# Performance work log

Measured on AMD Instinct MI355X. Metric: run time of the kernel, lower is better.

The kernel has to match this reference:

```python
import jax, jax.numpy as jnp
import numpy as np


def setup_inputs() -> dict:
    key = jax.random.key(0)
    ks = jax.random.split(key, 8)
    B, N, M, H = 8192, 2048, 2048, 10
    return {
        "X": jax.random.normal(ks[0], (B, N), dtype=jnp.float32),
        "weight": jax.random.normal(ks[1], (N, M), dtype=jnp.float32),
        "W1": jax.random.normal(ks[2], (3, H), dtype=jnp.float32) * 0.5,
        "b1": jax.random.normal(ks[3], (H,), dtype=jnp.float32) * 0.1,
        "W2": jax.random.normal(ks[4], (H, H), dtype=jnp.float32) * 0.3,
        "b2": jax.random.normal(ks[5], (H,), dtype=jnp.float32) * 0.1,
        "W3": jax.random.normal(ks[6], (H, 1), dtype=jnp.float32) * 0.3,
        "b3": jax.random.normal(ks[7], (1,), dtype=jnp.float32) * 0.1,
    }


def reference(X, weight, W1, b1, W2, b2, W3, b3):
    # NCA local rule, vectorized over all (i, j) cells.
    # 'forward'  = mean of column j excluding row i  (leave-one-out col mean)
    # 'backward' = mean of row i excluding column j  (leave-one-out row mean)
    n, m = weight.shape
    col_sum = jnp.sum(weight, axis=0, keepdims=True)            # [1, m]
    row_sum = jnp.sum(weight, axis=1, keepdims=True)            # [n, 1]
    fwd_mean = (col_sum - weight) / jnp.float32(n - 1)          # [n, m]
    bwd_mean = (row_sum - weight) / jnp.float32(m - 1)          # [n, m]
    feats = jnp.stack([weight, fwd_mean, bwd_mean], axis=-1)    # [n, m, 3]
    # tiny 3 -> 10 -> 10 -> 1 MLP applied per cell
    h = jax.nn.relu(feats @ W1 + b1)                            # [n, m, 10]
    h = jax.nn.relu(h @ W2 + b2)                                # [n, m, 10]
    updates = (h @ W3 + b3)[..., 0]                             # [n, m]
    new_weight = weight + updates
    # forward: softmax(X @ W)
    return jax.nn.softmax(X @ new_weight, axis=-1)
```

## Files before the change

### kernel.cpp

```cpp
#include <hip/hip_runtime.h>
#include <hip/hip_bf16.h>


typedef int int4v __attribute__((ext_vector_type(4)));
typedef int int16v __attribute__((ext_vector_type(16)));

#define GK 2048
#define NROWS 2048
#define MCOLS 2048
#define NCHUNK 16

#define CS_BLOCKS 128
#define RS_BLOCKS 2048
__global__ __launch_bounds__(256) void pre_kernel(
    const float* __restrict__ X, const float* __restrict__ W,
    signed char* __restrict__ X1, signed char* __restrict__ X2,
    float* __restrict__ sx1,
    float* __restrict__ part, float* __restrict__ rowS) {
  const int bid = blockIdx.x;
  const int tid = threadIdx.x;

  if (bid < CS_BLOCKS) {
    int chunk = bid >> 3;
    int j = (bid & 7) * 256 + tid;
    int i0 = chunk * (NROWS / NCHUNK);
    float s = 0.f;
    for (int i = i0; i < i0 + NROWS / NCHUNK; ++i) s += W[(size_t)i * MCOLS + j];
    part[(size_t)chunk * MCOLS + j] = s;
    return;
  }
  if (bid < CS_BLOCKS + RS_BLOCKS) {
    int row = bid - CS_BLOCKS;
    const float4* p = (const float4*)(W + (size_t)row * MCOLS);
    float4 a = p[tid];
    float4 b = p[tid + 256];
    float v = (a.x + a.y) + (a.z + a.w) + (b.x + b.y) + (b.z + b.w);
    __shared__ float red[256];
    red[tid] = v;
    __syncthreads();
    for (int s = 128; s > 0; s >>= 1) {
      if (tid < s) red[tid] += red[tid + s];
      __syncthreads();
    }
    if (tid == 0) rowS[row] = red[0];
    return;
  }
  {
    int row = bid - CS_BLOCKS - RS_BLOCKS;
    const float4* xr = (const float4*)(X + (size_t)row * GK);
    float4 a = xr[tid * 2];
    float4 b = xr[tid * 2 + 1];
    float xs[8] = {a.x, a.y, a.z, a.w, b.x, b.y, b.z, b.w};
    float am = 0.f;
#pragma unroll
    for (int i = 0; i < 8; ++i) am = fmaxf(am, fabsf(xs[i]));
    const int lane = tid & 63, wv = tid >> 6;
#pragma unroll
    for (int off = 32; off > 0; off >>= 1)
      am = fmaxf(am, __shfl_xor(am, off));
    __shared__ float wred[4];
    if (lane == 0) wred[wv] = am;
    __syncthreads();
    float amax = fmaxf(fmaxf(wred[0], wred[1]), fmaxf(wred[2], wred[3]));
    float s1 = amax * (1.0f / 127.0f);
    float inv = 127.0f / amax;
    int q1[8], q2[8];
#pragma unroll
    for (int i = 0; i < 8; ++i) {
      q1[i] = (int)rintf(xs[i] * inv);
      float r = xs[i] - (float)q1[i] * s1;
      q2[i] = (int)rintf(r * (254.0f * inv));
    }
    unsigned lo1 = (q1[0] & 255) | ((q1[1] & 255) << 8) | ((q1[2] & 255) << 16) | ((q1[3] & 255) << 24);
    unsigned hi1 = (q1[4] & 255) | ((q1[5] & 255) << 8) | ((q1[6] & 255) << 16) | ((q1[7] & 255) << 24);
    unsigned lo2 = (q2[0] & 255) | ((q2[1] & 255) << 8) | ((q2[2] & 255) << 16) | ((q2[3] & 255) << 24);
    unsigned hi2 = (q2[4] & 255) | ((q2[5] & 255) << 8) | ((q2[6] & 255) << 16) | ((q2[7] & 255) << 24);
    ((uint2*)(X1 + (size_t)row * GK))[tid] = make_uint2(lo1, hi1);
    ((uint2*)(X2 + (size_t)row * GK))[tid] = make_uint2(lo2, hi2);
    if (tid == 0) sx1[row] = s1;
  }
}

__global__ __launch_bounds__(256) void nca_update_kernel(
    const float* __restrict__ W, const float* __restrict__ part,
    const float* __restrict__ rowS,
    const float* __restrict__ W1, const float* __restrict__ b1,
    const float* __restrict__ W2, const float* __restrict__ b2,
    const float* __restrict__ W3, const float* __restrict__ b3,
    float* __restrict__ Wt) {
  __shared__ float sW1[30], sb1[10], sW2[100], sb2[10], sW3[10], sb3;
  __shared__ float sColS[32];
  __shared__ float cred[NCHUNK][33];
  __shared__ float Tf[32][33];
  const int tid = threadIdx.x;
  const int i0 = blockIdx.y * 32;
  const int j0 = blockIdx.x * 32;

  if (tid < 30) sW1[tid] = W1[tid];
  if (tid < 10) { sb1[tid] = b1[tid]; sb2[tid] = b2[tid]; sW3[tid] = W3[tid]; }
  if (tid >= 32 && tid < 132) sW2[tid - 32] = W2[tid - 32];
  if (tid == 0) sb3 = b3[0];

  {
    int ch = tid >> 5;
    int jl = tid & 31;
    cred[ch][jl]     = part[(size_t)ch * MCOLS + j0 + jl];
    cred[ch + 8][jl] = part[(size_t)(ch + 8) * MCOLS + j0 + jl];
  }
  __syncthreads();
  if (tid < 32) {
    float s = 0.f;
#pragma unroll
    for (int c = 0; c < NCHUNK; ++c) s += cred[c][tid];
    sColS[tid] = s;
  }
  __syncthreads();

  const int r = tid >> 5;
  const int c = tid & 31;

  float w[4], fwd[4], bwd[4];
#pragma unroll
  for (int cell = 0; cell < 4; ++cell) {
    int il = r + 8 * cell;
    float wv = W[(size_t)(i0 + il) * MCOLS + j0 + c];
    w[cell] = wv;
    fwd[cell] = (sColS[c] - wv) * (1.0f / (float)(NROWS - 1));
    bwd[cell] = (rowS[i0 + il] - wv) * (1.0f / (float)(MCOLS - 1));
  }

  float h1[4][10];
#pragma unroll
  for (int o = 0; o < 10; ++o) {
    float w1a = sW1[o], w1b = sW1[10 + o], w1c = sW1[20 + o], bb = sb1[o];
#pragma unroll
    for (int cell = 0; cell < 4; ++cell) {
      float v = fmaf(w[cell], w1a, fmaf(fwd[cell], w1b, fmaf(bwd[cell], w1c, bb)));
      h1[cell][o] = fmaxf(v, 0.f);
    }
  }
  float u[4] = {sb3, sb3, sb3, sb3};
#pragma unroll
  for (int o = 0; o < 10; ++o) {
    float h2[4];
    float bb = sb2[o];
#pragma unroll
    for (int cell = 0; cell < 4; ++cell) h2[cell] = bb;
#pragma unroll
    for (int p = 0; p < 10; ++p) {
      float wv = sW2[p * 10 + o];
#pragma unroll
      for (int cell = 0; cell < 4; ++cell) h2[cell] = fmaf(h1[cell][p], wv, h2[cell]);
    }
    float w3 = sW3[o];
#pragma unroll
    for (int cell = 0; cell < 4; ++cell) u[cell] = fmaf(fmaxf(h2[cell], 0.f), w3, u[cell]);
  }

#pragma unroll
  for (int cell = 0; cell < 4; ++cell) {
    int il = r + 8 * cell;
    Tf[il][c] = w[cell] + u[cell];
  }
  __syncthreads();

  {
    int r2 = tid >> 4;
    int ic = (tid & 15) * 2;
#pragma unroll
    for (int half = 0; half < 2; ++half) {
      int jl = r2 + 16 * half;
      float2 v = make_float2(Tf[ic][jl], Tf[ic + 1][jl]);
      *(float2*)(&Wt[(size_t)(j0 + jl) * NROWS + i0 + ic]) = v;
    }
  }
}

__global__ __launch_bounds__(256) void bquant_kernel(
    const float* __restrict__ Wt, signed char* __restrict__ B1,
    signed char* __restrict__ B2, float* __restrict__ sw1) {
  const int row = blockIdx.x;
  const int tid = threadIdx.x;
  const float4* wr = (const float4*)(Wt + (size_t)row * GK);
  float4 a = wr[tid * 2];
  float4 b = wr[tid * 2 + 1];
  float xs[8] = {a.x, a.y, a.z, a.w, b.x, b.y, b.z, b.w};
  float am = 0.f;
#pragma unroll
  for (int i = 0; i < 8; ++i) am = fmaxf(am, fabsf(xs[i]));
  const int lane = tid & 63, wv = tid >> 6;
#pragma unroll
  for (int off = 32; off > 0; off >>= 1)
    am = fmaxf(am, __shfl_xor(am, off));
  __shared__ float wred[4];
  if (lane == 0) wred[wv] = am;
  __syncthreads();
  float amax = fmaxf(fmaxf(wred[0], wred[1]), fmaxf(wred[2], wred[3]));
  float s1 = amax * (1.0f / 127.0f);
  float inv = 127.0f / amax;
  int q1[8], q2[8];
#pragma unroll
  for (int i = 0; i < 8; ++i) {
    q1[i] = (int)rintf(xs[i] * inv);
    float r = xs[i] - (float)q1[i] * s1;
    q2[i] = (int)rintf(r * (254.0f * inv));
  }
  unsigned lo1 = (q1[0] & 255) | ((q1[1] & 255) << 8) | ((q1[2] & 255) << 16) | ((q1[3] & 255) << 24);
  unsigned hi1 = (q1[4] & 255) | ((q1[5] & 255) << 8) | ((q1[6] & 255) << 16) | ((q1[7] & 255) << 24);
  unsigned lo2 = (q2[0] & 255) | ((q2[1] & 255) << 8) | ((q2[2] & 255) << 16) | ((q2[3] & 255) << 24);
  unsigned hi2 = (q2[4] & 255) | ((q2[5] & 255) << 8) | ((q2[6] & 255) << 16) | ((q2[7] & 255) << 24);
  ((uint2*)(B1 + (size_t)row * GK))[tid] = make_uint2(lo1, hi1);
  ((uint2*)(B2 + (size_t)row * GK))[tid] = make_uint2(lo2, hi2);
  if (tid == 0) sw1[row] = s1;
}

__global__ __launch_bounds__(256, 2) void gemm_kernel(
    const signed char* __restrict__ X1, const signed char* __restrict__ X2,
    const signed char* __restrict__ B1, const signed char* __restrict__ B2,
    const float* __restrict__ sw1, float* __restrict__ C) {
  __shared__ __align__(16) char sL[32768];

  const int tid = threadIdx.x;
  const int lane = tid & 63;
  const int wave = tid >> 6;
  const int wr = wave >> 1;
  const int wc = wave & 1;

  const int bx = blockIdx.x;
  const int by = blockIdx.y;

  const signed char* A1g = X1 + (size_t)(by * 128) * GK;
  const signed char* A2g = X2 + (size_t)(by * 128) * GK;
  const signed char* B1g = B1 + (size_t)(bx * 128) * GK;
  const signed char* B2g = B2 + (size_t)(bx * 128) * GK;

  const int srow = lane >> 2;
  const int skof = ((lane & 3) ^ ((lane >> 3) & 3)) * 16;

  const int rl = lane & 15;
  const int fhalf = (lane >> 4) & 1;
  const int fck = lane >> 5;

  int aoff[2][2], boff[2][2];
#pragma unroll
  for (int t = 0; t < 2; ++t)
#pragma unroll
    for (int ks = 0; ks < 2; ++ks) {
      int c = 2 * ks + fck;
      int slot = 4 * rl + (c ^ ((rl >> 1) & 3));
      aoff[t][ks] = (wr * 4 + t * 2 + fhalf) * 1024 + slot * 16;
      boff[t][ks] = (wc * 4 + t * 2 + fhalf) * 1024 + slot * 16;
    }

  int16v acc_h[2][2], acc_c[2][2];
#pragma unroll
  for (int i = 0; i < 2; ++i)
#pragma unroll
    for (int j = 0; j < 2; ++j)
#pragma unroll
      for (int e = 0; e < 16; ++e) { acc_h[i][j][e] = 0; acc_c[i][j][e] = 0; }

  for (int k0 = 0; k0 < GK; k0 += 64) {
#pragma unroll
    for (int r = 0; r < 2; ++r) {
      int R = wave * 2 + r;
      size_t goff = (size_t)(R * 16 + srow) * GK + k0 + skof;
      int ldsoff = R * 1024;
      __builtin_amdgcn_global_load_lds(
          (const __attribute__((address_space(1))) void*)(A1g + goff),
          (__attribute__((address_space(3))) void*)(sL + ldsoff), 16, 0, 0);
      __builtin_amdgcn_global_load_lds(
          (const __attribute__((address_space(1))) void*)(A2g + goff),
          (__attribute__((address_space(3))) void*)(sL + 8192 + ldsoff), 16, 0, 0);
      __builtin_amdgcn_global_load_lds(
          (const __attribute__((address_space(1))) void*)(B1g + goff),
          (__attribute__((address_space(3))) void*)(sL + 16384 + ldsoff), 16, 0, 0);
      __builtin_amdgcn_global_load_lds(
          (const __attribute__((address_space(1))) void*)(B2g + goff),
          (__attribute__((address_space(3))) void*)(sL + 24576 + ldsoff), 16, 0, 0);
    }
    __syncthreads();

    int4v a1[2][2], a2[2][2];
#pragma unroll
    for (int mi = 0; mi < 2; ++mi)
#pragma unroll
      for (int ks = 0; ks < 2; ++ks) {
        a1[mi][ks] = *(const int4v*)(sL + aoff[mi][ks]);
        a2[mi][ks] = *(const int4v*)(sL + 8192 + aoff[mi][ks]);
      }
#pragma unroll
    for (int ni = 0; ni < 2; ++ni)
#pragma unroll
      for (int ks = 0; ks < 2; ++ks) {
        int4v b1f = *(const int4v*)(sL + 16384 + boff[ni][ks]);
        int4v b2f = *(const int4v*)(sL + 24576 + boff[ni][ks]);
#pragma unroll
        for (int mi = 0; mi < 2; ++mi) {
          acc_h[mi][ni] = __builtin_amdgcn_mfma_i32_32x32x32_i8(a1[mi][ks], b1f, acc_h[mi][ni], 0, 0, 0);
          acc_c[mi][ni] = __builtin_amdgcn_mfma_i32_32x32x32_i8(a1[mi][ks], b2f, acc_c[mi][ni], 0, 0, 0);
          acc_c[mi][ni] = __builtin_amdgcn_mfma_i32_32x32x32_i8(a2[mi][ks], b1f, acc_c[mi][ni], 0, 0, 0);
        }
      }
    __syncthreads();
  }

  const int ecol = lane & 31;
  const int erow = 4 * (lane >> 5);
#pragma unroll
  for (int ni = 0; ni < 2; ++ni) {
    int col = bx * 128 + wc * 64 + ni * 32 + ecol;
    float sw = sw1[col];
#pragma unroll
    for (int mi = 0; mi < 2; ++mi) {
#pragma unroll
      for (int reg = 0; reg < 16; ++reg) {
        int row = by * 128 + wr * 64 + mi * 32 + (reg & 3) + 8 * (reg >> 2) + erow;
        float v = (float)acc_h[mi][ni][reg] + (float)acc_c[mi][ni][reg] * (1.0f / 254.0f);
        C[(size_t)row * 2048 + col] = v * sw;
      }
    }
  }
}

__global__ __launch_bounds__(256) void softmax_kernel(
    float* __restrict__ C, const float* __restrict__ sx1) {
  const int lane = threadIdx.x & 63;
  const int wv = threadIdx.x >> 6;
  const int row = blockIdx.x * 4 + wv;
  const float sx = sx1[row];
  float4* p = (float4*)(C + (size_t)row * MCOLS);

  float4 v[8];
#pragma unroll
  for (int j = 0; j < 8; ++j) {
    v[j] = p[j * 64 + lane];
    v[j].x *= sx; v[j].y *= sx; v[j].z *= sx; v[j].w *= sx;
  }

  float vmax = -3.4e38f;
#pragma unroll
  for (int j = 0; j < 8; ++j)
    vmax = fmaxf(vmax, fmaxf(fmaxf(v[j].x, v[j].y), fmaxf(v[j].z, v[j].w)));
#pragma unroll
  for (int off = 32; off > 0; off >>= 1)
    vmax = fmaxf(vmax, __shfl_xor(vmax, off));

  float sum = 0.f;
#pragma unroll
  for (int j = 0; j < 8; ++j) {
    v[j].x = __expf(v[j].x - vmax);
    v[j].y = __expf(v[j].y - vmax);
    v[j].z = __expf(v[j].z - vmax);
    v[j].w = __expf(v[j].w - vmax);
    sum += (v[j].x + v[j].y) + (v[j].z + v[j].w);
  }
#pragma unroll
  for (int off = 32; off > 0; off >>= 1)
    sum += __shfl_xor(sum, off);
  float inv = 1.0f / sum;

#pragma unroll
  for (int j = 0; j < 8; ++j) {
    v[j].x *= inv; v[j].y *= inv; v[j].z *= inv; v[j].w *= inv;
    p[j * 64 + lane] = v[j];
  }
}

extern "C" void kernel_launch(void* const* d_in, const int* in_sizes, int n_in,
                              void* d_out, int out_size, void* d_ws, size_t ws_size,
                              hipStream_t stream) {
  const float* X      = (const float*)d_in[0];
  const float* weight = (const float*)d_in[1];
  const float* W1     = (const float*)d_in[2];
  const float* b1     = (const float*)d_in[3];
  const float* W2     = (const float*)d_in[4];
  const float* b2     = (const float*)d_in[5];
  const float* W3     = (const float*)d_in[6];
  const float* b3     = (const float*)d_in[7];
  float* out = (float*)d_out;

  const int N = 2048, M = 2048;
  const int Bdim = in_sizes[0] / N;

  float* rowS = (float*)d_ws;
  float* part = rowS + 2048;
  float* sx1  = part + NCHUNK * 2048;
  float* sw1  = sx1 + 8192;
  float* Wt   = sw1 + 2048;
  signed char* X1 = (signed char*)(Wt + (size_t)M * N);
  signed char* X2 = X1 + (size_t)Bdim * N;
  signed char* B1q = X2 + (size_t)Bdim * N;
  signed char* B2q = B1q + (size_t)M * N;

  pre_kernel<<<CS_BLOCKS + RS_BLOCKS + Bdim, 256, 0, stream>>>(
      X, weight, X1, X2, sx1, part, rowS);

  nca_update_kernel<<<dim3(M / 32, N / 32), 256, 0, stream>>>(
      weight, part, rowS, W1, b1, W2, b2, W3, b3, Wt);

  bquant_kernel<<<M, 256, 0, stream>>>(Wt, B1q, B2q, sw1);

  gemm_kernel<<<dim3(M / 128, Bdim / 128), 256, 0, stream>>>(
      X1, X2, B1q, B2q, sw1, out);

  softmax_kernel<<<Bdim / 4, 256, 0, stream>>>(out, sx1);
}
```

Baseline: 289.3 us.

## Restructure int8 GEMM into 256x128 tiles with triple-buffered LDS prefetch

The GEMM block grows to 512 threads and a 256x128 output tile. The single-buffer load-then-compute loop becomes a three-stage LDS ring that prefetches two K-steps ahead, with global loads interleaved between MFMA quadrants and s_setprio raised around the MFMA groups. The aim is to hide global-to-LDS latency behind compute and to reuse each B tile across more rows. In exchange it uses 144KB of LDS per block, which limits occupancy, and it relies on hand-placed waitcnt and barrier sequencing that must be exactly right.

```diff
diff --git a/kernel.cpp b/kernel.cpp
--- a/kernel.cpp
+++ b/kernel.cpp
@@ -214,11 +214,39 @@
   if (tid == 0) sw1[row] = s1;
 }
 
-__global__ __launch_bounds__(256, 2) void gemm_kernel(
+#define BM 256
+#define BN 128
+#define BK 64
+#define NT (GK / BK)
+#define BUFSZ 49152
+
+__device__ __forceinline__ void glds16(const signed char* g, char* l) {
+  __builtin_amdgcn_global_load_lds(
+      (const __attribute__((address_space(1))) void*)g,
+      (__attribute__((address_space(3))) void*)l, 16, 0, 0);
+}
+
+#define QUAD(mi, ni)                                                           \
+  {                                                                            \
+    acc_h[mi][ni] = __builtin_amdgcn_mfma_i32_32x32x32_i8(                     \
+        a1f[mi][0], b1f[ni][0], acc_h[mi][ni], 0, 0, 0);                       \
+    acc_c[mi][ni] = __builtin_amdgcn_mfma_i32_32x32x32_i8(                     \
+        a1f[mi][0], b2f[ni][0], acc_c[mi][ni], 0, 0, 0);                       \
+    acc_c[mi][ni] = __builtin_amdgcn_mfma_i32_32x32x32_i8(                     \
+        a2f[mi][0], b1f[ni][0], acc_c[mi][ni], 0, 0, 0);                       \
+    acc_h[mi][ni] = __builtin_amdgcn_mfma_i32_32x32x32_i8(                     \
+        a1f[mi][1], b1f[ni][1], acc_h[mi][ni], 0, 0, 0);                       \
+    acc_c[mi][ni] = __builtin_amdgcn_mfma_i32_32x32x32_i8(                     \
+        a1f[mi][1], b2f[ni][1], acc_c[mi][ni], 0, 0, 0);                       \
+    acc_c[mi][ni] = __builtin_amdgcn_mfma_i32_32x32x32_i8(                     \
+        a2f[mi][1], b1f[ni][1], acc_c[mi][ni], 0, 0, 0);                       \
+  }
+
+__global__ __launch_bounds__(512, 2) void gemm_kernel(
     const signed char* __restrict__ X1, const signed char* __restrict__ X2,
     const signed char* __restrict__ B1, const signed char* __restrict__ B2,
     const float* __restrict__ sw1, float* __restrict__ C) {
-  __shared__ __align__(16) char sL[32768];
+  __shared__ __align__(16) char sL[3 * BUFSZ];
 
   const int tid = threadIdx.x;
   const int lane = tid & 63;
@@ -229,27 +257,28 @@
   const int bx = blockIdx.x;
   const int by = blockIdx.y;
 
-  const signed char* A1g = X1 + (size_t)(by * 128) * GK;
-  const signed char* A2g = X2 + (size_t)(by * 128) * GK;
-  const signed char* B1g = B1 + (size_t)(bx * 128) * GK;
-  const signed char* B2g = B2 + (size_t)(bx * 128) * GK;
+  const signed char* A1g = X1 + (size_t)(by * BM) * GK;
+  const signed char* A2g = X2 + (size_t)(by * BM) * GK;
+  const signed char* B1g = B1 + (size_t)(bx * BN) * GK;
+  const signed char* B2g = B2 + (size_t)(bx * BN) * GK;
 
   const int srow = lane >> 2;
-  const int skof = ((lane & 3) ^ ((lane >> 3) & 3)) * 16;
+  const int schk = (lane & 3) ^ ((lane >> 3) & 3);
+  const size_t qoff = (size_t)(wave * 16 + srow) * GK + schk * 16;
+  const int wds = wave * 1024;
 
   const int rl = lane & 15;
-  const int fhalf = (lane >> 4) & 1;
-  const int fck = lane >> 5;
-
+  const int bhalf = (lane >> 4) & 1;
+  const int kck = lane >> 5;
   int aoff[2][2], boff[2][2];
 #pragma unroll
-  for (int t = 0; t < 2; ++t)
+  for (int mi = 0; mi < 2; ++mi)
 #pragma unroll
     for (int ks = 0; ks < 2; ++ks) {
-      int c = 2 * ks + fck;
+      int c = 2 * ks + kck;
       int slot = 4 * rl + (c ^ ((rl >> 1) & 3));
-      aoff[t][ks] = (wr * 4 + t * 2 + fhalf) * 1024 + slot * 16;
-      boff[t][ks] = (wc * 4 + t * 2 + fhalf) * 1024 + slot * 16;
+      aoff[mi][ks] = (wr * 4 + mi * 2 + bhalf) * 1024 + slot * 16;
+      boff[mi][ks] = 32768 + (wc * 4 + mi * 2 + bhalf) * 1024 + slot * 16;
     }
 
   int16v acc_h[2][2], acc_c[2][2];
@@ -260,64 +289,103 @@
 #pragma unroll
       for (int e = 0; e < 16; ++e) { acc_h[i][j][e] = 0; acc_c[i][j][e] = 0; }
 
-  for (int k0 = 0; k0 < GK; k0 += 64) {
-#pragma unroll
-    for (int r = 0; r < 2; ++r) {
-      int R = wave * 2 + r;
-      size_t goff = (size_t)(R * 16 + srow) * GK + k0 + skof;
-      int ldsoff = R * 1024;
-      __builtin_amdgcn_global_load_lds(
-          (const __attribute__((address_space(1))) void*)(A1g + goff),
-          (__attribute__((address_space(3))) void*)(sL + ldsoff), 16, 0, 0);
-      __builtin_amdgcn_global_load_lds(
-          (const __attribute__((address_space(1))) void*)(A2g + goff),
-          (__attribute__((address_space(3))) void*)(sL + 8192 + ldsoff), 16, 0, 0);
-      __builtin_amdgcn_global_load_lds(
-          (const __attribute__((address_space(1))) void*)(B1g + goff),
-          (__attribute__((address_space(3))) void*)(sL + 16384 + ldsoff), 16, 0, 0);
-      __builtin_amdgcn_global_load_lds(
-          (const __attribute__((address_space(1))) void*)(B2g + goff),
-          (__attribute__((address_space(3))) void*)(sL + 24576 + ldsoff), 16, 0, 0);
-    }
-    __syncthreads();
-
-    int4v a1[2][2], a2[2][2];
-#pragma unroll
-    for (int mi = 0; mi < 2; ++mi)
-#pragma unroll
-      for (int ks = 0; ks < 2; ++ks) {
-        a1[mi][ks] = *(const int4v*)(sL + aoff[mi][ks]);
-        a2[mi][ks] = *(const int4v*)(sL + 8192 + aoff[mi][ks]);
-      }
-#pragma unroll
-    for (int ni = 0; ni < 2; ++ni)
-#pragma unroll
-      for (int ks = 0; ks < 2; ++ks) {
-        int4v b1f = *(const int4v*)(sL + 16384 + boff[ni][ks]);
-        int4v b2f = *(const int4v*)(sL + 24576 + boff[ni][ks]);
-#pragma unroll
-        for (int mi = 0; mi < 2; ++mi) {
-          acc_h[mi][ni] = __builtin_amdgcn_mfma_i32_32x32x32_i8(a1[mi][ks], b1f, acc_h[mi][ni], 0, 0, 0);
-          acc_c[mi][ni] = __builtin_amdgcn_mfma_i32_32x32x32_i8(a1[mi][ks], b2f, acc_c[mi][ni], 0, 0, 0);
-          acc_c[mi][ni] = __builtin_amdgcn_mfma_i32_32x32x32_i8(a2[mi][ks], b1f, acc_c[mi][ni], 0, 0, 0);
-        }
-      }
-    __syncthreads();
+#pragma unroll
+  for (int t = 0; t < 2; ++t) {
+    char* wb = sL + t * BUFSZ;
+    const size_t k0 = (size_t)t * BK;
+    glds16(A1g + qoff + k0, wb + wds);
+    glds16(A1g + qoff + (size_t)128 * GK + k0, wb + 8192 + wds);
+    glds16(A2g + qoff + k0, wb + 16384 + wds);
+    glds16(A2g + qoff + (size_t)128 * GK + k0, wb + 24576 + wds);
+    glds16(B1g + qoff + k0, wb + 32768 + wds);
+    glds16(B2g + qoff + k0, wb + 40960 + wds);
+  }
+
+  const char* sbuf = sL;
+  char* wbuf = sL + 2 * BUFSZ;
+
+  int4v a1f[2][2], a2f[2][2], b1f[2][2], b2f[2][2];
+
+#pragma unroll 1
+  for (int kt = 0; kt < NT; ++kt) {
+    if (kt + 1 < NT) asm volatile("s_waitcnt vmcnt(6)" ::: "memory");
+    else             asm volatile("s_waitcnt vmcnt(0)" ::: "memory");
+    __builtin_amdgcn_s_barrier();
+
+    const size_t k2 = (size_t)(kt + 2) * BK;
+    const bool pf = (kt + 2 < NT);
+
+#pragma unroll
+    for (int ks = 0; ks < 2; ++ks) {
+      a1f[0][ks] = *(const int4v*)(sbuf + aoff[0][ks]);
+      a2f[0][ks] = *(const int4v*)(sbuf + aoff[0][ks] + 16384);
+      b1f[0][ks] = *(const int4v*)(sbuf + boff[0][ks]);
+      b2f[0][ks] = *(const int4v*)(sbuf + boff[0][ks] + 8192);
+    }
+    if (pf) {
+      glds16(A1g + qoff + k2, wbuf + wds);
+      glds16(A1g + qoff + (size_t)128 * GK + k2, wbuf + 8192 + wds);
+    }
+    __builtin_amdgcn_s_barrier();
+    asm volatile("s_waitcnt lgkmcnt(0)" ::: "memory");
+    __builtin_amdgcn_s_setprio(1);
+    QUAD(0, 0);
+    __builtin_amdgcn_s_setprio(0);
+    __builtin_amdgcn_s_barrier();
+
+#pragma unroll
+    for (int ks = 0; ks < 2; ++ks) {
+      b1f[1][ks] = *(const int4v*)(sbuf + boff[1][ks]);
+      b2f[1][ks] = *(const int4v*)(sbuf + boff[1][ks] + 8192);
+    }
+    if (pf) {
+      glds16(A2g + qoff + k2, wbuf + 16384 + wds);
+      glds16(A2g + qoff + (size_t)128 * GK + k2, wbuf + 24576 + wds);
+    }
+    __builtin_amdgcn_s_barrier();
+    asm volatile("s_waitcnt lgkmcnt(0)" ::: "memory");
+    __builtin_amdgcn_s_setprio(1);
+    QUAD(0, 1);
+    __builtin_amdgcn_s_setprio(0);
+    __builtin_amdgcn_s_barrier();
+
+#pragma unroll
+    for (int ks = 0; ks < 2; ++ks) {
+      a1f[1][ks] = *(const int4v*)(sbuf + aoff[1][ks]);
+      a2f[1][ks] = *(const int4v*)(sbuf + aoff[1][ks] + 16384);
+    }
+    if (pf) {
+      glds16(B1g + qoff + k2, wbuf + 32768 + wds);
+      glds16(B2g + qoff + k2, wbuf + 40960 + wds);
+    }
+    __builtin_amdgcn_s_barrier();
+    asm volatile("s_waitcnt lgkmcnt(0)" ::: "memory");
+    __builtin_amdgcn_s_setprio(1);
+    QUAD(1, 1);
+    __builtin_amdgcn_s_setprio(0);
+    __builtin_amdgcn_s_barrier();
+
+    __builtin_amdgcn_s_setprio(1);
+    QUAD(1, 0);
+    __builtin_amdgcn_s_setprio(0);
+
+    sbuf += BUFSZ; if (sbuf == sL + 3 * BUFSZ) sbuf = sL;
+    wbuf += BUFSZ; if (wbuf == sL + 3 * BUFSZ) wbuf = sL;
   }
 
   const int ecol = lane & 31;
   const int erow = 4 * (lane >> 5);
 #pragma unroll
   for (int ni = 0; ni < 2; ++ni) {
-    int col = bx * 128 + wc * 64 + ni * 32 + ecol;
+    int col = bx * BN + wc * 64 + ni * 32 + ecol;
     float sw = sw1[col];
 #pragma unroll
     for (int mi = 0; mi < 2; ++mi) {
 #pragma unroll
       for (int reg = 0; reg < 16; ++reg) {
-        int row = by * 128 + wr * 64 + mi * 32 + (reg & 3) + 8 * (reg >> 2) + erow;
+        int row = by * BM + wr * 64 + mi * 32 + (reg & 3) + 8 * (reg >> 2) + erow;
         float v = (float)acc_h[mi][ni][reg] + (float)acc_c[mi][ni][reg] * (1.0f / 254.0f);
-        C[(size_t)row * 2048 + col] = v * sw;
+        C[(size_t)row * MCOLS + col] = v * sw;
       }
     }
   }
@@ -401,7 +469,7 @@
 
   bquant_kernel<<<M, 256, 0, stream>>>(Wt, B1q, B2q, sw1);
 
-  gemm_kernel<<<dim3(M / 128, Bdim / 128), 256, 0, stream>>>(
+  gemm_kernel<<<dim3(M / BN, Bdim / BM), 512, 0, stream>>>(
       X1, X2, B1q, B2q, sw1, out);
 
   softmax_kernel<<<Bdim / 4, 256, 0, stream>>>(out, sx1);
```

Measured after the change: 288.7 us. About the same (-0.2%).

## Pipeline int8 GEMM with 4-stage LDS ring and register double-buffered fragments

Applied to the files above, without the earlier changes.

The int8 split-precision GEMM becomes a software pipeline. A 4-buffer LDS ring keeps tiles prefetched three K-steps ahead with direct global-to-LDS loads, one barrier per step and explicit vmcnt/lgkmcnt waits. Register fragments are double-buffered so the next step's ds_reads overlap the current MFMAs, and each wave loads one of the four operand streams. This costs 128KB of LDS and one block per CU instead of two. The NCA update kernel also reads the MLP weights directly from global memory instead of staging them in shared memory.

```diff
diff --git a/kernel.cpp b/kernel.cpp
--- a/kernel.cpp
+++ b/kernel.cpp
@@ -88,7 +88,6 @@
     const float* __restrict__ W2, const float* __restrict__ b2,
     const float* __restrict__ W3, const float* __restrict__ b3,
     float* __restrict__ Wt) {
-  __shared__ float sW1[30], sb1[10], sW2[100], sb2[10], sW3[10], sb3;
   __shared__ float sColS[32];
   __shared__ float cred[NCHUNK][33];
   __shared__ float Tf[32][33];
@@ -96,11 +95,6 @@
   const int i0 = blockIdx.y * 32;
   const int j0 = blockIdx.x * 32;
 
-  if (tid < 30) sW1[tid] = W1[tid];
-  if (tid < 10) { sb1[tid] = b1[tid]; sb2[tid] = b2[tid]; sW3[tid] = W3[tid]; }
-  if (tid >= 32 && tid < 132) sW2[tid - 32] = W2[tid - 32];
-  if (tid == 0) sb3 = b3[0];
-
   {
     int ch = tid >> 5;
     int jl = tid & 31;
@@ -132,27 +126,28 @@
   float h1[4][10];
 #pragma unroll
   for (int o = 0; o < 10; ++o) {
-    float w1a = sW1[o], w1b = sW1[10 + o], w1c = sW1[20 + o], bb = sb1[o];
+    float w1a = W1[o], w1b = W1[10 + o], w1c = W1[20 + o], bb = b1[o];
 #pragma unroll
     for (int cell = 0; cell < 4; ++cell) {
       float v = fmaf(w[cell], w1a, fmaf(fwd[cell], w1b, fmaf(bwd[cell], w1c, bb)));
       h1[cell][o] = fmaxf(v, 0.f);
     }
   }
-  float u[4] = {sb3, sb3, sb3, sb3};
+  const float b3v = b3[0];
+  float u[4] = {b3v, b3v, b3v, b3v};
 #pragma unroll
   for (int o = 0; o < 10; ++o) {
     float h2[4];
-    float bb = sb2[o];
+    float bb = b2[o];
 #pragma unroll
     for (int cell = 0; cell < 4; ++cell) h2[cell] = bb;
 #pragma unroll
     for (int p = 0; p < 10; ++p) {
-      float wv = sW2[p * 10 + o];
+      float wv = W2[p * 10 + o];
 #pragma unroll
       for (int cell = 0; cell < 4; ++cell) h2[cell] = fmaf(h1[cell][p], wv, h2[cell]);
     }
-    float w3 = sW3[o];
+    float w3 = W3[o];
 #pragma unroll
     for (int cell = 0; cell < 4; ++cell) u[cell] = fmaf(fmaxf(h2[cell], 0.f), w3, u[cell]);
   }
@@ -214,11 +209,99 @@
   if (tid == 0) sw1[row] = s1;
 }
 
-__global__ __launch_bounds__(256, 2) void gemm_kernel(
+#define BM 128
+#define BN 128
+#define BK 64
+#define NT (GK / BK)
+#define BUFSZ 32768
+#define SROWSZ ((size_t)16 * GK)
+
+__device__ __forceinline__ void glds16(const signed char* g, char* l) {
+  __builtin_amdgcn_global_load_lds(
+      (const __attribute__((address_space(1))) void*)g,
+      (__attribute__((address_space(3))) void*)l, 16, 0, 0);
+}
+
+__device__ __forceinline__ int4v ds_read128(const char* p) {
+  int4v r;
+  asm volatile("ds_read_b128 %0, %1"
+               : "=v"(r)
+               : "v"((const __attribute__((address_space(3))) char*)p));
+  return r;
+}
+
+#define MFMA_I8 __builtin_amdgcn_mfma_i32_32x32x32_i8
+
+#define RD16(NX, rb_)                                                          \
+  NX##a1[0][0] = ds_read128((rb_) + aoff[0][0]);                               \
+  NX##a1[0][1] = ds_read128((rb_) + aoff[0][1]);                               \
+  NX##a1[1][0] = ds_read128((rb_) + aoff[1][0]);                               \
+  NX##a1[1][1] = ds_read128((rb_) + aoff[1][1]);                               \
+  NX##a2[0][0] = ds_read128((rb_) + aoff[0][0] + 8192);                        \
+  NX##a2[0][1] = ds_read128((rb_) + aoff[0][1] + 8192);                        \
+  NX##a2[1][0] = ds_read128((rb_) + aoff[1][0] + 8192);                        \
+  NX##a2[1][1] = ds_read128((rb_) + aoff[1][1] + 8192);                        \
+  NX##b1[0][0] = ds_read128((rb_) + boff[0][0]);                               \
+  NX##b1[0][1] = ds_read128((rb_) + boff[0][1]);                               \
+  NX##b1[1][0] = ds_read128((rb_) + boff[1][0]);                               \
+  NX##b1[1][1] = ds_read128((rb_) + boff[1][1]);                               \
+  NX##b2[0][0] = ds_read128((rb_) + boff[0][0] + 8192);                        \
+  NX##b2[0][1] = ds_read128((rb_) + boff[0][1] + 8192);                        \
+  NX##b2[1][0] = ds_read128((rb_) + boff[1][0] + 8192);                        \
+  NX##b2[1][1] = ds_read128((rb_) + boff[1][1] + 8192);
+
+#define MM12(CUR, ks)                                                          \
+  acc_h[0][0] = MFMA_I8(CUR##a1[0][ks], CUR##b1[0][ks], acc_h[0][0], 0, 0, 0); \
+  acc_h[0][1] = MFMA_I8(CUR##a1[0][ks], CUR##b1[1][ks], acc_h[0][1], 0, 0, 0); \
+  acc_h[1][0] = MFMA_I8(CUR##a1[1][ks], CUR##b1[0][ks], acc_h[1][0], 0, 0, 0); \
+  acc_h[1][1] = MFMA_I8(CUR##a1[1][ks], CUR##b1[1][ks], acc_h[1][1], 0, 0, 0); \
+  acc_c[0][0] = MFMA_I8(CUR##a1[0][ks], CUR##b2[0][ks], acc_c[0][0], 0, 0, 0); \
+  acc_c[0][1] = MFMA_I8(CUR##a1[0][ks], CUR##b2[1][ks], acc_c[0][1], 0, 0, 0); \
+  acc_c[1][0] = MFMA_I8(CUR##a1[1][ks], CUR##b2[0][ks], acc_c[1][0], 0, 0, 0); \
+  acc_c[1][1] = MFMA_I8(CUR##a1[1][ks], CUR##b2[1][ks], acc_c[1][1], 0, 0, 0); \
+  acc_c[0][0] = MFMA_I8(CUR##a2[0][ks], CUR##b1[0][ks], acc_c[0][0], 0, 0, 0); \
+  acc_c[0][1] = MFMA_I8(CUR##a2[0][ks], CUR##b1[1][ks], acc_c[0][1], 0, 0, 0); \
+  acc_c[1][0] = MFMA_I8(CUR##a2[1][ks], CUR##b1[0][ks], acc_c[1][0], 0, 0, 0); \
+  acc_c[1][1] = MFMA_I8(CUR##a2[1][ks], CUR##b1[1][ks], acc_c[1][1], 0, 0, 0);
+
+#define STAGE8(wb_, gp_)                                                       \
+  glds16((gp_) + 0 * SROWSZ, (wb_) + 0 * 1024 + lane * 16);                    \
+  glds16((gp_) + 1 * SROWSZ, (wb_) + 1 * 1024 + lane * 16);                    \
+  glds16((gp_) + 2 * SROWSZ, (wb_) + 2 * 1024 + lane * 16);                    \
+  glds16((gp_) + 3 * SROWSZ, (wb_) + 3 * 1024 + lane * 16);                    \
+  glds16((gp_) + 4 * SROWSZ, (wb_) + 4 * 1024 + lane * 16);                    \
+  glds16((gp_) + 5 * SROWSZ, (wb_) + 5 * 1024 + lane * 16);                    \
+  glds16((gp_) + 6 * SROWSZ, (wb_) + 6 * 1024 + lane * 16);                    \
+  glds16((gp_) + 7 * SROWSZ, (wb_) + 7 * 1024 + lane * 16);
+
+#define STEP(i, CUR, NXT)                                                      \
+  {                                                                            \
+    if ((i) + 2 < NT) asm volatile("s_waitcnt vmcnt(8)" ::: "memory");         \
+    else              asm volatile("s_waitcnt vmcnt(0)" ::: "memory");         \
+    __builtin_amdgcn_s_barrier();                                              \
+    if ((i) + 1 < NT) {                                                        \
+      const char* rb_ = sL + (((i) + 1) & 3) * BUFSZ;                          \
+      RD16(NXT, rb_);                                                          \
+    }                                                                          \
+    if ((i) + 3 < NT) {                                                        \
+      char* wb_ = sL + (((i) + 3) & 3) * BUFSZ + wave * 8192;                  \
+      const signed char* gp_ = gw + (size_t)((i) + 3) * BK;                    \
+      STAGE8(wb_, gp_);                                                        \
+    }                                                                          \
+    if ((i) + 1 < NT) asm volatile("s_waitcnt lgkmcnt(15)" ::: "memory");      \
+    else              asm volatile("s_waitcnt lgkmcnt(0)" ::: "memory");       \
+    __builtin_amdgcn_sched_barrier(0);                                         \
+    __builtin_amdgcn_s_setprio(1);                                             \
+    MM12(CUR, 0);                                                              \
+    MM12(CUR, 1);                                                              \
+    __builtin_amdgcn_s_setprio(0);                                             \
+  }
+
+__global__ __launch_bounds__(256, 1) void gemm_kernel(
     const signed char* __restrict__ X1, const signed char* __restrict__ X2,
     const signed char* __restrict__ B1, const signed char* __restrict__ B2,
     const float* __restrict__ sw1, float* __restrict__ C) {
-  __shared__ __align__(16) char sL[32768];
+  __shared__ __align__(16) char sL[4 * BUFSZ];
 
   const int tid = threadIdx.x;
   const int lane = tid & 63;
@@ -229,27 +312,29 @@
   const int bx = blockIdx.x;
   const int by = blockIdx.y;
 
-  const signed char* A1g = X1 + (size_t)(by * 128) * GK;
-  const signed char* A2g = X2 + (size_t)(by * 128) * GK;
-  const signed char* B1g = B1 + (size_t)(bx * 128) * GK;
-  const signed char* B2g = B2 + (size_t)(bx * 128) * GK;
+  const signed char* A1g = X1 + (size_t)(by * BM) * GK;
+  const signed char* A2g = X2 + (size_t)(by * BM) * GK;
+  const signed char* B1g = B1 + (size_t)(bx * BN) * GK;
+  const signed char* B2g = B2 + (size_t)(bx * BN) * GK;
 
   const int srow = lane >> 2;
-  const int skof = ((lane & 3) ^ ((lane >> 3) & 3)) * 16;
+  const int schk = (lane & 3) ^ ((lane >> 3) & 3);
+  const signed char* gw =
+      (wave == 0 ? A1g : wave == 1 ? A2g : wave == 2 ? B1g : B2g) +
+      (size_t)srow * GK + schk * 16;
 
   const int rl = lane & 15;
   const int fhalf = (lane >> 4) & 1;
   const int fck = lane >> 5;
-
   int aoff[2][2], boff[2][2];
 #pragma unroll
-  for (int t = 0; t < 2; ++t)
+  for (int mi = 0; mi < 2; ++mi)
 #pragma unroll
     for (int ks = 0; ks < 2; ++ks) {
       int c = 2 * ks + fck;
       int slot = 4 * rl + (c ^ ((rl >> 1) & 3));
-      aoff[t][ks] = (wr * 4 + t * 2 + fhalf) * 1024 + slot * 16;
-      boff[t][ks] = (wc * 4 + t * 2 + fhalf) * 1024 + slot * 16;
+      aoff[mi][ks] = (wr * 4 + mi * 2 + fhalf) * 1024 + slot * 16;
+      boff[mi][ks] = 16384 + (wc * 4 + mi * 2 + fhalf) * 1024 + slot * 16;
     }
 
   int16v acc_h[2][2], acc_c[2][2];
@@ -260,64 +345,38 @@
 #pragma unroll
       for (int e = 0; e < 16; ++e) { acc_h[i][j][e] = 0; acc_c[i][j][e] = 0; }
 
-  for (int k0 = 0; k0 < GK; k0 += 64) {
-#pragma unroll
-    for (int r = 0; r < 2; ++r) {
-      int R = wave * 2 + r;
-      size_t goff = (size_t)(R * 16 + srow) * GK + k0 + skof;
-      int ldsoff = R * 1024;
-      __builtin_amdgcn_global_load_lds(
-          (const __attribute__((address_space(1))) void*)(A1g + goff),
-          (__attribute__((address_space(3))) void*)(sL + ldsoff), 16, 0, 0);
-      __builtin_amdgcn_global_load_lds(
-          (const __attribute__((address_space(1))) void*)(A2g + goff),
-          (__attribute__((address_space(3))) void*)(sL + 8192 + ldsoff), 16, 0, 0);
-      __builtin_amdgcn_global_load_lds(
-          (const __attribute__((address_space(1))) void*)(B1g + goff),
-          (__attribute__((address_space(3))) void*)(sL + 16384 + ldsoff), 16, 0, 0);
-      __builtin_amdgcn_global_load_lds(
-          (const __attribute__((address_space(1))) void*)(B2g + goff),
-          (__attribute__((address_space(3))) void*)(sL + 24576 + ldsoff), 16, 0, 0);
-    }
-    __syncthreads();
-
-    int4v a1[2][2], a2[2][2];
-#pragma unroll
-    for (int mi = 0; mi < 2; ++mi)
-#pragma unroll
-      for (int ks = 0; ks < 2; ++ks) {
-        a1[mi][ks] = *(const int4v*)(sL + aoff[mi][ks]);
-        a2[mi][ks] = *(const int4v*)(sL + 8192 + aoff[mi][ks]);
-      }
-#pragma unroll
-    for (int ni = 0; ni < 2; ++ni)
-#pragma unroll
-      for (int ks = 0; ks < 2; ++ks) {
-        int4v b1f = *(const int4v*)(sL + 16384 + boff[ni][ks]);
-        int4v b2f = *(const int4v*)(sL + 24576 + boff[ni][ks]);
-#pragma unroll
-        for (int mi = 0; mi < 2; ++mi) {
-          acc_h[mi][ni] = __builtin_amdgcn_mfma_i32_32x32x32_i8(a1[mi][ks], b1f, acc_h[mi][ni], 0, 0, 0);
-          acc_c[mi][ni] = __builtin_amdgcn_mfma_i32_32x32x32_i8(a1[mi][ks], b2f, acc_c[mi][ni], 0, 0, 0);
-          acc_c[mi][ni] = __builtin_amdgcn_mfma_i32_32x32x32_i8(a2[mi][ks], b1f, acc_c[mi][ni], 0, 0, 0);
-        }
-      }
-    __syncthreads();
+  int4v s0_a1[2][2], s0_a2[2][2], s0_b1[2][2], s0_b2[2][2];
+  int4v s1_a1[2][2], s1_a2[2][2], s1_b1[2][2], s1_b2[2][2];
+
+#pragma unroll
+  for (int t = 0; t < 3; ++t) {
+    char* wb = sL + t * BUFSZ + wave * 8192;
+    const signed char* gp = gw + (size_t)t * BK;
+    STAGE8(wb, gp);
+  }
+  asm volatile("s_waitcnt vmcnt(16)" ::: "memory");
+  __builtin_amdgcn_s_barrier();
+  RD16(s0_, sL);
+
+#pragma unroll 1
+  for (int i = 0; i < NT; i += 2) {
+    STEP(i, s0_, s1_);
+    STEP(i + 1, s1_, s0_);
   }
 
   const int ecol = lane & 31;
   const int erow = 4 * (lane >> 5);
 #pragma unroll
   for (int ni = 0; ni < 2; ++ni) {
-    int col = bx * 128 + wc * 64 + ni * 32 + ecol;
+    int col = bx * BN + wc * 64 + ni * 32 + ecol;
     float sw = sw1[col];
 #pragma unroll
     for (int mi = 0; mi < 2; ++mi) {
 #pragma unroll
       for (int reg = 0; reg < 16; ++reg) {
-        int row = by * 128 + wr * 64 + mi * 32 + (reg & 3) + 8 * (reg >> 2) + erow;
+        int row = by * BM + wr * 64 + mi * 32 + (reg & 3) + 8 * (reg >> 2) + erow;
         float v = (float)acc_h[mi][ni][reg] + (float)acc_c[mi][ni][reg] * (1.0f / 254.0f);
-        C[(size_t)row * 2048 + col] = v * sw;
+        C[(size_t)row * MCOLS + col] = v * sw;
       }
     }
   }
@@ -401,7 +460,7 @@
 
   bquant_kernel<<<M, 256, 0, stream>>>(Wt, B1q, B2q, sw1);
 
-  gemm_kernel<<<dim3(M / 128, Bdim / 128), 256, 0, stream>>>(
+  gemm_kernel<<<dim3(M / BN, Bdim / BM), 256, 0, stream>>>(
       X1, X2, B1q, B2q, sw1, out);
 
   softmax_kernel<<<Bdim / 4, 256, 0, stream>>>(out, sx1);
```

Result: slower. 317.5 us (+9.8%).

## Pre-swizzle int8 operands into MFMA fragment layout and stream GEMM from registers

Applied to the files above, without the earlier changes.

The quantization kernels now handle one row per wave and write int8 data directly in MFMA-fragment order. The GEMM can then load its operands straight from global memory into registers with a double-buffered register prefetch, with no LDS staging or barriers. The GEMM tile grows to 256x128 with 512 threads, and the NCA kernel reads the MLP weights directly instead of staging them in shared memory. Without LDS, operand reuse across waves now relies on L2/L1 caching, which may raise global memory traffic.

```diff
diff --git a/kernel.cpp b/kernel.cpp
--- a/kernel.cpp
+++ b/kernel.cpp
@@ -46,38 +46,48 @@
     return;
   }
   {
-    int row = bid - CS_BLOCKS - RS_BLOCKS;
-    const float4* xr = (const float4*)(X + (size_t)row * GK);
-    float4 a = xr[tid * 2];
-    float4 b = xr[tid * 2 + 1];
-    float xs[8] = {a.x, a.y, a.z, a.w, b.x, b.y, b.z, b.w};
+    int rb = bid - CS_BLOCKS - RS_BLOCKS;
+    const int lane = tid & 63, wv = tid >> 6;
+    const int row = rb * 4 + wv;
+    const float4* xr = (const float4*)(X + (size_t)row * GK) + lane * 8;
+    float xs[32];
+#pragma unroll
+    for (int i = 0; i < 8; ++i) {
+      float4 t = xr[i];
+      xs[i * 4 + 0] = t.x; xs[i * 4 + 1] = t.y;
+      xs[i * 4 + 2] = t.z; xs[i * 4 + 3] = t.w;
+    }
     float am = 0.f;
 #pragma unroll
-    for (int i = 0; i < 8; ++i) am = fmaxf(am, fabsf(xs[i]));
-    const int lane = tid & 63, wv = tid >> 6;
+    for (int i = 0; i < 32; ++i) am = fmaxf(am, fabsf(xs[i]));
 #pragma unroll
     for (int off = 32; off > 0; off >>= 1)
       am = fmaxf(am, __shfl_xor(am, off));
-    __shared__ float wred[4];
-    if (lane == 0) wred[wv] = am;
-    __syncthreads();
-    float amax = fmaxf(fmaxf(wred[0], wred[1]), fmaxf(wred[2], wred[3]));
-    float s1 = amax * (1.0f / 127.0f);
-    float inv = 127.0f / amax;
-    int q1[8], q2[8];
-#pragma unroll
-    for (int i = 0; i < 8; ++i) {
-      q1[i] = (int)rintf(xs[i] * inv);
-      float r = xs[i] - (float)q1[i] * s1;
-      q2[i] = (int)rintf(r * (254.0f * inv));
-    }
-    unsigned lo1 = (q1[0] & 255) | ((q1[1] & 255) << 8) | ((q1[2] & 255) << 16) | ((q1[3] & 255) << 24);
-    unsigned hi1 = (q1[4] & 255) | ((q1[5] & 255) << 8) | ((q1[6] & 255) << 16) | ((q1[7] & 255) << 24);
-    unsigned lo2 = (q2[0] & 255) | ((q2[1] & 255) << 8) | ((q2[2] & 255) << 16) | ((q2[3] & 255) << 24);
-    unsigned hi2 = (q2[4] & 255) | ((q2[5] & 255) << 8) | ((q2[6] & 255) << 16) | ((q2[7] & 255) << 24);
-    ((uint2*)(X1 + (size_t)row * GK))[tid] = make_uint2(lo1, hi1);
-    ((uint2*)(X2 + (size_t)row * GK))[tid] = make_uint2(lo2, hi2);
-    if (tid == 0) sx1[row] = s1;
+    float s1 = am * (1.0f / 127.0f);
+    float inv = 127.0f / am;
+    unsigned w1[8], w2[8];
+#pragma unroll
+    for (int i = 0; i < 8; ++i) { w1[i] = 0u; w2[i] = 0u; }
+#pragma unroll
+    for (int i = 0; i < 32; ++i) {
+      int q1 = (int)rintf(xs[i] * inv);
+      float r = xs[i] - (float)q1 * s1;
+      int q2 = (int)rintf(r * (254.0f * inv));
+      w1[i >> 2] |= (unsigned)(q1 & 255) << ((i & 3) * 8);
+      w2[i >> 2] |= (unsigned)(q2 & 255) << ((i & 3) * 8);
+    }
+    const int m32 = row >> 5, ml = row & 31;
+    int4v* d1 = (int4v*)X1 + ((size_t)m32 * 64 + lane) * 64;
+    int4v* d2 = (int4v*)X2 + ((size_t)m32 * 64 + lane) * 64;
+    int4v v1lo = {(int)w1[0], (int)w1[1], (int)w1[2], (int)w1[3]};
+    int4v v1hi = {(int)w1[4], (int)w1[5], (int)w1[6], (int)w1[7]};
+    int4v v2lo = {(int)w2[0], (int)w2[1], (int)w2[2], (int)w2[3]};
+    int4v v2hi = {(int)w2[4], (int)w2[5], (int)w2[6], (int)w2[7]};
+    d1[ml]      = v1lo;
+    d1[ml + 32] = v1hi;
+    d2[ml]      = v2lo;
+    d2[ml + 32] = v2hi;
+    if (lane == 0) sx1[row] = s1;
   }
 }
 
@@ -88,7 +98,6 @@
     const float* __restrict__ W2, const float* __restrict__ b2,
     const float* __restrict__ W3, const float* __restrict__ b3,
     float* __restrict__ Wt) {
-  __shared__ float sW1[30], sb1[10], sW2[100], sb2[10], sW3[10], sb3;
   __shared__ float sColS[32];
   __shared__ float cred[NCHUNK][33];
   __shared__ float Tf[32][33];
@@ -96,11 +105,6 @@
   const int i0 = blockIdx.y * 32;
   const int j0 = blockIdx.x * 32;
 
-  if (tid < 30) sW1[tid] = W1[tid];
-  if (tid < 10) { sb1[tid] = b1[tid]; sb2[tid] = b2[tid]; sW3[tid] = W3[tid]; }
-  if (tid >= 32 && tid < 132) sW2[tid - 32] = W2[tid - 32];
-  if (tid == 0) sb3 = b3[0];
-
   {
     int ch = tid >> 5;
     int jl = tid & 31;
@@ -132,27 +136,28 @@
   float h1[4][10];
 #pragma unroll
   for (int o = 0; o < 10; ++o) {
-    float w1a = sW1[o], w1b = sW1[10 + o], w1c = sW1[20 + o], bb = sb1[o];
+    float w1a = W1[o], w1b = W1[10 + o], w1c = W1[20 + o], bb = b1[o];
 #pragma unroll
     for (int cell = 0; cell < 4; ++cell) {
       float v = fmaf(w[cell], w1a, fmaf(fwd[cell], w1b, fmaf(bwd[cell], w1c, bb)));
       h1[cell][o] = fmaxf(v, 0.f);
     }
   }
-  float u[4] = {sb3, sb3, sb3, sb3};
+  const float b3v = b3[0];
+  float u[4] = {b3v, b3v, b3v, b3v};
 #pragma unroll
   for (int o = 0; o < 10; ++o) {
     float h2[4];
-    float bb = sb2[o];
+    float bb = b2[o];
 #pragma unroll
     for (int cell = 0; cell < 4; ++cell) h2[cell] = bb;
 #pragma unroll
     for (int p = 0; p < 10; ++p) {
-      float wv = sW2[p * 10 + o];
+      float wv = W2[p * 10 + o];
 #pragma unroll
       for (int cell = 0; cell < 4; ++cell) h2[cell] = fmaf(h1[cell][p], wv, h2[cell]);
     }
-    float w3 = sW3[o];
+    float w3 = W3[o];
 #pragma unroll
     for (int cell = 0; cell < 4; ++cell) u[cell] = fmaf(fmaxf(h2[cell], 0.f), w3, u[cell]);
   }
@@ -179,47 +184,83 @@
 __global__ __launch_bounds__(256) void bquant_kernel(
     const float* __restrict__ Wt, signed char* __restrict__ B1,
     signed char* __restrict__ B2, float* __restrict__ sw1) {
-  const int row = blockIdx.x;
   const int tid = threadIdx.x;
-  const float4* wr = (const float4*)(Wt + (size_t)row * GK);
-  float4 a = wr[tid * 2];
-  float4 b = wr[tid * 2 + 1];
-  float xs[8] = {a.x, a.y, a.z, a.w, b.x, b.y, b.z, b.w};
+  const int lane = tid & 63, wv = tid >> 6;
+  const int row = blockIdx.x * 4 + wv;
+  const float4* wr = (const float4*)(Wt + (size_t)row * GK) + lane * 8;
+  float xs[32];
+#pragma unroll
+  for (int i = 0; i < 8; ++i) {
+    float4 t = wr[i];
+    xs[i * 4 + 0] = t.x; xs[i * 4 + 1] = t.y;
+    xs[i * 4 + 2] = t.z; xs[i * 4 + 3] = t.w;
+  }
   float am = 0.f;
 #pragma unroll
-  for (int i = 0; i < 8; ++i) am = fmaxf(am, fabsf(xs[i]));
-  const int lane = tid & 63, wv = tid >> 6;
+  for (int i = 0; i < 32; ++i) am = fmaxf(am, fabsf(xs[i]));
 #pragma unroll
   for (int off = 32; off > 0; off >>= 1)
     am = fmaxf(am, __shfl_xor(am, off));
-  __shared__ float wred[4];
-  if (lane == 0) wred[wv] = am;
-  __syncthreads();
-  float amax = fmaxf(fmaxf(wred[0], wred[1]), fmaxf(wred[2], wred[3]));
-  float s1 = amax * (1.0f / 127.0f);
-  float inv = 127.0f / amax;
-  int q1[8], q2[8];
-#pragma unroll
-  for (int i = 0; i < 8; ++i) {
-    q1[i] = (int)rintf(xs[i] * inv);
-    float r = xs[i] - (float)q1[i] * s1;
-    q2[i] = (int)rintf(r * (254.0f * inv));
-  }
-  unsigned lo1 = (q1[0] & 255) | ((q1[1] & 255) << 8) | ((q1[2] & 255) << 16) | ((q1[3] & 255) << 24);
-  unsigned hi1 = (q1[4] & 255) | ((q1[5] & 255) << 8) | ((q1[6] & 255) << 16) | ((q1[7] & 255) << 24);
-  unsigned lo2 = (q2[0] & 255) | ((q2[1] & 255) << 8) | ((q2[2] & 255) << 16) | ((q2[3] & 255) << 24);
-  unsigned hi2 = (q2[4] & 255) | ((q2[5] & 255) << 8) | ((q2[6] & 255) << 16) | ((q2[7] & 255) << 24);
-  ((uint2*)(B1 + (size_t)row * GK))[tid] = make_uint2(lo1, hi1);
-  ((uint2*)(B2 + (size_t)row * GK))[tid] = make_uint2(lo2, hi2);
-  if (tid == 0) sw1[row] = s1;
-}
-
-__global__ __launch_bounds__(256, 2) void gemm_kernel(
-    const signed char* __restrict__ X1, const signed char* __restrict__ X2,
-    const signed char* __restrict__ B1, const signed char* __restrict__ B2,
+  float s1 = am * (1.0f / 127.0f);
+  float inv = 127.0f / am;
+  unsigned w1[8], w2[8];
+#pragma unroll
+  for (int i = 0; i < 8; ++i) { w1[i] = 0u; w2[i] = 0u; }
+#pragma unroll
+  for (int i = 0; i < 32; ++i) {
+    int q1 = (int)rintf(xs[i] * inv);
+    float r = xs[i] - (float)q1 * s1;
+    int q2 = (int)rintf(r * (254.0f * inv));
+    w1[i >> 2] |= (unsigned)(q1 & 255) << ((i & 3) * 8);
+    w2[i >> 2] |= (unsigned)(q2 & 255) << ((i & 3) * 8);
+  }
+  const int n32 = row >> 5, nl = row & 31;
+  int4v* d1 = (int4v*)B1 + ((size_t)n32 * 64 + lane) * 64;
+  int4v* d2 = (int4v*)B2 + ((size_t)n32 * 64 + lane) * 64;
+  int4v v1lo = {(int)w1[0], (int)w1[1], (int)w1[2], (int)w1[3]};
+  int4v v1hi = {(int)w1[4], (int)w1[5], (int)w1[6], (int)w1[7]};
+  int4v v2lo = {(int)w2[0], (int)w2[1], (int)w2[2], (int)w2[3]};
+  int4v v2hi = {(int)w2[4], (int)w2[5], (int)w2[6], (int)w2[7]};
+  d1[nl]      = v1lo;
+  d1[nl + 32] = v1hi;
+  d2[nl]      = v2lo;
+  d2[nl + 32] = v2hi;
+  if (lane == 0) sw1[row] = s1;
+}
+
+#define BM 256
+#define BN 128
+
+#define MFMA_I8 __builtin_amdgcn_mfma_i32_32x32x32_i8
+
+#define LOADT(S, k)                                                            \
+  S##a1_0 = A1p[a0 + (size_t)(k) * 64];                                        \
+  S##a1_1 = A1p[a1 + (size_t)(k) * 64];                                        \
+  S##a2_0 = A2p[a0 + (size_t)(k) * 64];                                        \
+  S##a2_1 = A2p[a1 + (size_t)(k) * 64];                                        \
+  S##b1_0 = B1p[b0 + (size_t)(k) * 64];                                        \
+  S##b1_1 = B1p[b1 + (size_t)(k) * 64];                                        \
+  S##b2_0 = B2p[b0 + (size_t)(k) * 64];                                        \
+  S##b2_1 = B2p[b1 + (size_t)(k) * 64];
+
+#define MM12S(S)                                                               \
+  acc_h[0][0] = MFMA_I8(S##a1_0, S##b1_0, acc_h[0][0], 0, 0, 0);               \
+  acc_h[0][1] = MFMA_I8(S##a1_0, S##b1_1, acc_h[0][1], 0, 0, 0);               \
+  acc_h[1][0] = MFMA_I8(S##a1_1, S##b1_0, acc_h[1][0], 0, 0, 0);               \
+  acc_h[1][1] = MFMA_I8(S##a1_1, S##b1_1, acc_h[1][1], 0, 0, 0);               \
+  acc_c[0][0] = MFMA_I8(S##a1_0, S##b2_0, acc_c[0][0], 0, 0, 0);               \
+  acc_c[0][1] = MFMA_I8(S##a1_0, S##b2_1, acc_c[0][1], 0, 0, 0);               \
+  acc_c[1][0] = MFMA_I8(S##a1_1, S##b2_0, acc_c[1][0], 0, 0, 0);               \
+  acc_c[1][1] = MFMA_I8(S##a1_1, S##b2_1, acc_c[1][1], 0, 0, 0);               \
+  acc_c[0][0] = MFMA_I8(S##a2_0, S##b1_0, acc_c[0][0], 0, 0, 0);               \
+  acc_c[0][1] = MFMA_I8(S##a2_0, S##b1_1, acc_c[0][1], 0, 0, 0);               \
+  acc_c[1][0] = MFMA_I8(S##a2_1, S##b1_0, acc_c[1][0], 0, 0, 0);               \
+  acc_c[1][1] = MFMA_I8(S##a2_1, S##b1_1, acc_c[1][1], 0, 0, 0);
+
+__global__ __launch_bounds__(512, 2) void gemm_kernel(
+    const int4v* __restrict__ A1p, const int4v* __restrict__ A2p,
+    const int4v* __restrict__ B1p, const int4v* __restrict__ B2p,
     const float* __restrict__ sw1, float* __restrict__ C) {
-  __shared__ __align__(16) char sL[32768];
-
   const int tid = threadIdx.x;
   const int lane = tid & 63;
   const int wave = tid >> 6;
@@ -229,28 +270,10 @@
   const int bx = blockIdx.x;
   const int by = blockIdx.y;
 
-  const signed char* A1g = X1 + (size_t)(by * 128) * GK;
-  const signed char* A2g = X2 + (size_t)(by * 128) * GK;
-  const signed char* B1g = B1 + (size_t)(bx * 128) * GK;
-  const signed char* B2g = B2 + (size_t)(bx * 128) * GK;
-
-  const int srow = lane >> 2;
-  const int skof = ((lane & 3) ^ ((lane >> 3) & 3)) * 16;
-
-  const int rl = lane & 15;
-  const int fhalf = (lane >> 4) & 1;
-  const int fck = lane >> 5;
-
-  int aoff[2][2], boff[2][2];
-#pragma unroll
-  for (int t = 0; t < 2; ++t)
-#pragma unroll
-    for (int ks = 0; ks < 2; ++ks) {
-      int c = 2 * ks + fck;
-      int slot = 4 * rl + (c ^ ((rl >> 1) & 3));
-      aoff[t][ks] = (wr * 4 + t * 2 + fhalf) * 1024 + slot * 16;
-      boff[t][ks] = (wc * 4 + t * 2 + fhalf) * 1024 + slot * 16;
-    }
+  const size_t a0 = ((size_t)(by * 8 + wr * 2 + 0) * 64) * 64 + lane;
+  const size_t a1 = ((size_t)(by * 8 + wr * 2 + 1) * 64) * 64 + lane;
+  const size_t b0 = ((size_t)(bx * 4 + wc * 2 + 0) * 64) * 64 + lane;
+  const size_t b1 = ((size_t)(bx * 4 + wc * 2 + 1) * 64) * 64 + lane;
 
   int16v acc_h[2][2], acc_c[2][2];
 #pragma unroll
@@ -260,64 +283,34 @@
 #pragma unroll
       for (int e = 0; e < 16; ++e) { acc_h[i][j][e] = 0; acc_c[i][j][e] = 0; }
 
-  for (int k0 = 0; k0 < GK; k0 += 64) {
-#pragma unroll
-    for (int r = 0; r < 2; ++r) {
-      int R = wave * 2 + r;
-      size_t goff = (size_t)(R * 16 + srow) * GK + k0 + skof;
-      int ldsoff = R * 1024;
-      __builtin_amdgcn_global_load_lds(
-          (const __attribute__((address_space(1))) void*)(A1g + goff),
-          (__attribute__((address_space(3))) void*)(sL + ldsoff), 16, 0, 0);
-      __builtin_amdgcn_global_load_lds(
-          (const __attribute__((address_space(1))) void*)(A2g + goff),
-          (__attribute__((address_space(3))) void*)(sL + 8192 + ldsoff), 16, 0, 0);
-      __builtin_amdgcn_global_load_lds(
-          (const __attribute__((address_space(1))) void*)(B1g + goff),
-          (__attribute__((address_space(3))) void*)(sL + 16384 + ldsoff), 16, 0, 0);
-      __builtin_amdgcn_global_load_lds(
-          (const __attribute__((address_space(1))) void*)(B2g + goff),
-          (__attribute__((address_space(3))) void*)(sL + 24576 + ldsoff), 16, 0, 0);
-    }
-    __syncthreads();
-
-    int4v a1[2][2], a2[2][2];
-#pragma unroll
-    for (int mi = 0; mi < 2; ++mi)
-#pragma unroll
-      for (int ks = 0; ks < 2; ++ks) {
-        a1[mi][ks] = *(const int4v*)(sL + aoff[mi][ks]);
-        a2[mi][ks] = *(const int4v*)(sL + 8192 + aoff[mi][ks]);
-      }
-#pragma unroll
-    for (int ni = 0; ni < 2; ++ni)
-#pragma unroll
-      for (int ks = 0; ks < 2; ++ks) {
-        int4v b1f = *(const int4v*)(sL + 16384 + boff[ni][ks]);
-        int4v b2f = *(const int4v*)(sL + 24576 + boff[ni][ks]);
-#pragma unroll
-        for (int mi = 0; mi < 2; ++mi) {
-          acc_h[mi][ni] = __builtin_amdgcn_mfma_i32_32x32x32_i8(a1[mi][ks], b1f, acc_h[mi][ni], 0, 0, 0);
-          acc_c[mi][ni] = __builtin_amdgcn_mfma_i32_32x32x32_i8(a1[mi][ks], b2f, acc_c[mi][ni], 0, 0, 0);
-          acc_c[mi][ni] = __builtin_amdgcn_mfma_i32_32x32x32_i8(a2[mi][ks], b1f, acc_c[mi][ni], 0, 0, 0);
-        }
-      }
-    __syncthreads();
-  }
+  int4v Pa1_0, Pa1_1, Pa2_0, Pa2_1, Pb1_0, Pb1_1, Pb2_0, Pb2_1;
+  int4v Qa1_0, Qa1_1, Qa2_0, Qa2_1, Qb1_0, Qb1_1, Qb2_0, Qb2_1;
+
+  LOADT(P, 0);
+#pragma unroll 1
+  for (int k = 0; k < 62; k += 2) {
+    LOADT(Q, k + 1);
+    MM12S(P);
+    LOADT(P, k + 2);
+    MM12S(Q);
+  }
+  LOADT(Q, 63);
+  MM12S(P);
+  MM12S(Q);
 
   const int ecol = lane & 31;
   const int erow = 4 * (lane >> 5);
 #pragma unroll
   for (int ni = 0; ni < 2; ++ni) {
-    int col = bx * 128 + wc * 64 + ni * 32 + ecol;
+    int col = bx * BN + wc * 64 + ni * 32 + ecol;
     float sw = sw1[col];
 #pragma unroll
     for (int mi = 0; mi < 2; ++mi) {
 #pragma unroll
       for (int reg = 0; reg < 16; ++reg) {
-        int row = by * 128 + wr * 64 + mi * 32 + (reg & 3) + 8 * (reg >> 2) + erow;
+        int row = by * BM + wr * 64 + mi * 32 + (reg & 3) + 8 * (reg >> 2) + erow;
         float v = (float)acc_h[mi][ni][reg] + (float)acc_c[mi][ni][reg] * (1.0f / 254.0f);
-        C[(size_t)row * 2048 + col] = v * sw;
+        C[(size_t)row * MCOLS + col] = v * sw;
       }
     }
   }
@@ -393,16 +386,17 @@
   signed char* B1q = X2 + (size_t)Bdim * N;
   signed char* B2q = B1q + (size_t)M * N;
 
-  pre_kernel<<<CS_BLOCKS + RS_BLOCKS + Bdim, 256, 0, stream>>>(
+  pre_kernel<<<CS_BLOCKS + RS_BLOCKS + Bdim / 4, 256, 0, stream>>>(
       X, weight, X1, X2, sx1, part, rowS);
 
   nca_update_kernel<<<dim3(M / 32, N / 32), 256, 0, stream>>>(
       weight, part, rowS, W1, b1, W2, b2, W3, b3, Wt);
 
-  bquant_kernel<<<M, 256, 0, stream>>>(Wt, B1q, B2q, sw1);
-
-  gemm_kernel<<<dim3(M / 128, Bdim / 128), 256, 0, stream>>>(
-      X1, X2, B1q, B2q, sw1, out);
+  bquant_kernel<<<M / 4, 256, 0, stream>>>(Wt, B1q, B2q, sw1);
+
+  gemm_kernel<<<dim3(M / BN, Bdim / BM), 512, 0, stream>>>(
+      (const int4v*)X1, (const int4v*)X2, (const int4v*)B1q, (const int4v*)B2q,
+      sw1, out);
 
   softmax_kernel<<<Bdim / 4, 256, 0, stream>>>(out, sx1);
 }
```

Measured after the change: 325.6 us. 1.13x slower.
